# Kernel optimization log

Measured on AMD Instinct MI355X. Metric: run time of the kernel, lower is better.

## Reference

```python
import jax, jax.numpy as jnp
import numpy as np

RADIUS = 0.2
NSAMPLE = 32
GROUPS = 4
EPS = 1e-5


def group_norm(x, gamma, beta):
    # x: [B, C, *spatial]; normalize per (batch, group) over channels-in-group + spatial
    B, C = x.shape[0], x.shape[1]
    rest = x.shape[2:]
    xr = x.reshape(B, GROUPS, -1)
    mean = xr.mean(-1, keepdims=True)
    var = xr.var(-1, keepdims=True)
    xr = (xr - mean) * jax.lax.rsqrt(var + EPS)
    x = xr.reshape((B, C) + rest)
    bshape = (1, C) + (1,) * len(rest)
    return x * gamma.reshape(bshape) + beta.reshape(bshape)


def ball_query(pos_t):
    # pos_t: [B, N, 3] -> idx [B, N, NSAMPLE] (query points == all points)
    N = pos_t.shape[1]
    sq = jnp.sum(pos_t * pos_t, axis=-1)  # [B, N]
    d = sq[:, :, None] + sq[:, None, :] - 2.0 * jnp.einsum('bnc,bmc->bnm', pos_t, pos_t)
    ar = jnp.arange(N, dtype=jnp.int32)
    gi = jnp.where(d > RADIUS * RADIUS, N, ar[None, None, :])  # [B, S, N]
    gi = jnp.sort(gi, axis=-1)[:, :, :NSAMPLE]  # ascending in-ball indices first
    first = gi[:, :, :1]
    gi = jnp.where(gi == N, first, gi)  # pad with first neighbor
    return gi


def setup_inputs() -> dict:
    key = jax.random.key(0)
    ks = jax.random.split(key, 6)
    B, C, N = 2, 64, 4096
    M = 4 * C  # mid channels
    return {
        'x': jax.random.normal(ks[0], (B, C, N), jnp.float32),
        'pos': jax.random.uniform(ks[1], (B, 3, N), jnp.float32),
        'w1': jax.random.normal(ks[2], (M, C), jnp.float32) * 0.05,
        'b1': jnp.zeros((M,), jnp.float32),
        'g1': jnp.ones((M,), jnp.float32),
        'be1': jnp.zeros((M,), jnp.float32),
        'wd': 1.0 + jax.random.normal(ks[3], (M,), jnp.float32) * 0.05,
        'gd': jnp.ones((M,), jnp.float32),
        'bed': jnp.zeros((M,), jnp.float32),
        'w2': jax.random.normal(ks[4], (C, M), jnp.float32) * 0.05,
        'b2': jnp.zeros((C,), jnp.float32),
        'g2': jnp.ones((C,), jnp.float32),
        'be2': jnp.zeros((C,), jnp.float32),
    }


def reference(x, pos, w1, b1, g1, be1, wd, gd, bed, w2, b2, g2, be2):
    # x: [B, C, N], pos: [B, 3, N]
    pos_t = jnp.transpose(pos, (0, 2, 1))  # [B, N, 3]
    idx = ball_query(pos_t)  # [B, N, K]

    # conv1 (1x1) -> GroupNorm -> GELU
    h = jnp.einsum('mc,bcn->bmn', w1, x) + b1[None, :, None]
    h = jax.nn.gelu(group_norm(h, g1, be1), approximate=False)  # [B, M, N]

    # gather neighbors: feats [B, N, M] indexed by idx [B, N, K]
    feats = jnp.transpose(h, (0, 2, 1))
    grouped = jax.vmap(lambda f, i: f[i])(feats, idx)  # [B, N, K, M]
    grouped = jnp.transpose(grouped, (0, 3, 1, 2))  # [B, M, N, K]

    # depthwise 1x1 conv (per-channel scale, no bias) -> GroupNorm -> max-pool over K -> GELU
    grouped = grouped * wd[None, :, None, None]
    grouped = group_norm(grouped, gd, bed)
    h2 = jax.nn.gelu(jnp.max(grouped, axis=-1), approximate=False)  # [B, M, N]

    # conv2 (1x1) -> GroupNorm -> residual
    out = jnp.einsum('cm,bmn->bcn', w2, h2) + b2[None, :, None]
    out = group_norm(out, g2, be2)
    return out + x
```

## Files before the change

kernel.cpp:

```cpp
#include <hip/hip_runtime.h>
#include <hip/hip_fp16.h>
#include <math.h>

#define BB 2
#define CC 64
#define NN 4096
#define MM 256
#define KK 32
#define GG 4
#define EPSF 1e-5f

__device__ __forceinline__ float gelu_exact(float x) {
    return 0.5f * x * (1.0f + erff(x * 0.70710678118654752f));
}

__device__ __forceinline__ unsigned pkmax(unsigned a, unsigned b) {
    unsigned d;
    asm volatile("v_pk_max_f16 %0, %1, %2" : "=v"(d) : "v"(a), "v"(b));
    return d;
}
__device__ __forceinline__ unsigned pkmin(unsigned a, unsigned b) {
    unsigned d;
    asm volatile("v_pk_min_f16 %0, %1, %2" : "=v"(d) : "v"(a), "v"(b));
    return d;
}
__device__ __forceinline__ unsigned selpair(unsigned mx, unsigned mn, float g0, float g1) {
    unsigned lo = (g0 >= 0.f) ? (mx & 0x0000FFFFu) : (mn & 0x0000FFFFu);
    unsigned hi = (g1 >= 0.f) ? (mx & 0xFFFF0000u) : (mn & 0xFFFF0000u);
    return lo | hi;
}

__global__ void k_init(double* st) {
    int t = threadIdx.x;
    if (t < 48) st[t] = 0.0;
}

__global__ void k_mlp1(const float* __restrict__ x, const float* __restrict__ w1,
                       const float* __restrict__ b1, float* __restrict__ h, double* st1) {
    __shared__ float xs[64 * 128];
    __shared__ float w1t[64 * 32];
    __shared__ float r1[4], r2[4];

    int bx = blockIdx.x;
    int nt = bx & 31, mt = (bx >> 5) & 7, b = bx >> 8;
    int n0 = nt * 128, m0 = mt * 32;
    int t = threadIdx.x;

    {
        int nq = t & 31, ch = t >> 5;
        #pragma unroll
        for (int p = 0; p < 8; p++) {
            int c = p * 8 + ch;
            float4 v = *(const float4*)&x[((size_t)(b * CC + c)) * NN + n0 + nq * 4];
            *(float4*)&xs[c * 128 + nq * 4] = v;
        }
    }
    {
        #pragma unroll
        for (int p = 0; p < 2; p++) {
            int idx = p * 256 + t;
            int m = idx >> 4, cq = idx & 15;
            float4 v = *(const float4*)&w1[(m0 + m) * CC + cq * 4];
            w1t[(cq * 4 + 0) * 32 + m] = v.x;
            w1t[(cq * 4 + 1) * 32 + m] = v.y;
            w1t[(cq * 4 + 2) * 32 + m] = v.z;
            w1t[(cq * 4 + 3) * 32 + m] = v.w;
        }
    }
    __syncthreads();

    int nq = t & 31;
    int mseg = t >> 5;
    float o[4][4];
    #pragma unroll
    for (int i = 0; i < 4; i++)
        #pragma unroll
        for (int j = 0; j < 4; j++) o[i][j] = 0.f;

    for (int c = 0; c < 64; c++) {
        float4 xv = *(float4*)&xs[c * 128 + nq * 4];
        float4 wv = *(float4*)&w1t[c * 32 + mseg * 4];
        o[0][0] = fmaf(wv.x, xv.x, o[0][0]); o[0][1] = fmaf(wv.x, xv.y, o[0][1]);
        o[0][2] = fmaf(wv.x, xv.z, o[0][2]); o[0][3] = fmaf(wv.x, xv.w, o[0][3]);
        o[1][0] = fmaf(wv.y, xv.x, o[1][0]); o[1][1] = fmaf(wv.y, xv.y, o[1][1]);
        o[1][2] = fmaf(wv.y, xv.z, o[1][2]); o[1][3] = fmaf(wv.y, xv.w, o[1][3]);
        o[2][0] = fmaf(wv.z, xv.x, o[2][0]); o[2][1] = fmaf(wv.z, xv.y, o[2][1]);
        o[2][2] = fmaf(wv.z, xv.z, o[2][2]); o[2][3] = fmaf(wv.z, xv.w, o[2][3]);
        o[3][0] = fmaf(wv.w, xv.x, o[3][0]); o[3][1] = fmaf(wv.w, xv.y, o[3][1]);
        o[3][2] = fmaf(wv.w, xv.z, o[3][2]); o[3][3] = fmaf(wv.w, xv.w, o[3][3]);
    }

    float s1 = 0.f, s2 = 0.f;
    #pragma unroll
    for (int mi = 0; mi < 4; mi++) {
        int m = m0 + mseg * 4 + mi;
        float bv = b1[m];
        float4 r;
        r.x = o[mi][0] + bv; r.y = o[mi][1] + bv;
        r.z = o[mi][2] + bv; r.w = o[mi][3] + bv;
        *(float4*)&h[((size_t)(b * MM + m)) * NN + n0 + nq * 4] = r;
        s1 += r.x + r.y + r.z + r.w;
        s2 = fmaf(r.x, r.x, s2); s2 = fmaf(r.y, r.y, s2);
        s2 = fmaf(r.z, r.z, s2); s2 = fmaf(r.w, r.w, s2);
    }
    for (int off = 32; off; off >>= 1) {
        s1 += __shfl_down(s1, off, 64);
        s2 += __shfl_down(s2, off, 64);
    }
    int w = t >> 6, l = t & 63;
    if (l == 0) { r1[w] = s1; r2[w] = s2; }
    __syncthreads();
    if (t == 0) {
        float ts1 = r1[0] + r1[1] + r1[2] + r1[3];
        float ts2 = r2[0] + r2[1] + r2[2] + r2[3];
        int g = m0 >> 6;
        atomicAdd(&st1[(b * GG + g) * 2 + 0], (double)ts1);
        atomicAdd(&st1[(b * GG + g) * 2 + 1], (double)ts2);
    }
}

__global__ void k_gn1t(const float* __restrict__ h, const float* __restrict__ g1,
                       const float* __restrict__ be1, const float* __restrict__ wd,
                       const double* __restrict__ st1, __half* __restrict__ pH,
                       float* __restrict__ R) {
    int n0 = blockIdx.x * 64;
    int m0 = blockIdx.y * 64;
    int b  = blockIdx.z;
    int g  = m0 >> 6;
    double s1 = st1[(b * GG + g) * 2 + 0];
    double s2 = st1[(b * GG + g) * 2 + 1];
    const double cnt = 64.0 * 4096.0;
    double mean_d = s1 / cnt;
    double var_d  = s2 / cnt - mean_d * mean_d;
    float mean = (float)mean_d;
    float rstd = rsqrtf((float)var_d + EPSF);

    __shared__ float tile[64 * 65];
    int t = threadIdx.x;
    int nq = t & 15, mr = t >> 4;
    #pragma unroll
    for (int pp = 0; pp < 4; pp++) {
        int row = pp * 16 + mr;
        int m = m0 + row;
        float a = rstd * g1[m];
        float cc2 = be1[m] - mean * a;
        float wdm = wd[m];
        float4 hv = *(const float4*)&h[((size_t)(b * MM + m)) * NN + n0 + nq * 4];
        tile[row * 65 + nq * 4 + 0] = gelu_exact(fmaf(hv.x, a, cc2)) * wdm;
        tile[row * 65 + nq * 4 + 1] = gelu_exact(fmaf(hv.y, a, cc2)) * wdm;
        tile[row * 65 + nq * 4 + 2] = gelu_exact(fmaf(hv.z, a, cc2)) * wdm;
        tile[row * 65 + nq * 4 + 3] = gelu_exact(fmaf(hv.w, a, cc2)) * wdm;
    }
    __syncthreads();
    #pragma unroll
    for (int pp = 0; pp < 4; pp++) {
        int id = pp * 256 + t;
        int nl = id >> 4, mq = id & 15;
        float a0 = tile[(mq * 4 + 0) * 65 + nl];
        float a1 = tile[(mq * 4 + 1) * 65 + nl];
        float a2 = tile[(mq * 4 + 2) * 65 + nl];
        float a3 = tile[(mq * 4 + 3) * 65 + nl];
        __half2 hA = __float22half2_rn(make_float2(a0, a1));
        __half2 hB = __float22half2_rn(make_float2(a2, a3));
        uint2 st8;
        st8.x = *(unsigned*)&hA; st8.y = *(unsigned*)&hB;
        *(uint2*)((char*)pH + ((((size_t)(b * NN) + n0 + nl)) << 9) + (m0 + mq * 4) * 2) = st8;
        float2 fa = __half22float2(hA);
        float2 fb = __half22float2(hB);
        float t1 = fa.x + fa.y + fb.x + fb.y;
        float t2 = fa.x * fa.x + fa.y * fa.y + fb.x * fb.x + fb.y * fb.y;
        #pragma unroll
        for (int off = 8; off; off >>= 1) {
            t1 += __shfl_down(t1, off, 16);
            t2 += __shfl_down(t2, off, 16);
        }
        if ((t & 15) == 0) {
            float* rr = &R[((size_t)(b * NN) + n0 + nl) * 8];
            rr[g]     = t1;
            rr[4 + g] = t2;
        }
    }
}

__global__ void k_ballq(const float* __restrict__ pos, int* __restrict__ idx) {
    int wid  = blockIdx.x * 4 + (threadIdx.x >> 6);
    int lane = threadIdx.x & 63;
    int b = wid >> 12;
    int n = wid & 4095;
    const float* px = pos + b * 3 * NN;
    const float* py = px + NN;
    const float* pz = py + NN;
    float qx = px[n], qy = py[n], qz = pz[n];
    float qsq = qx*qx + qy*qy + qz*qz;
    int* row = idx + (b * NN + n) * KK;

    int found = 0;
    int first = -1;
    const float R2 = 0.04f;
    for (int m0 = 0; m0 < NN && found < KK; m0 += 64) {
        int m = m0 + lane;
        float ax = px[m], ay = py[m], az = pz[m];
        float msq = ax*ax + ay*ay + az*az;
        float dot = qx*ax + qy*ay + qz*az;
        float d = qsq + msq - 2.0f * dot;
        bool hit = !(d > R2);
        unsigned long long mask = __ballot(hit);
        if (first < 0 && mask) first = m0 + (__ffsll((long long)mask) - 1);
        unsigned long long lt = (lane == 0) ? 0ULL : (mask & ((1ULL << lane) - 1ULL));
        int posh = __popcll(lt);
        if (hit && (found + posh) < KK) row[found + posh] = m;
        found += __popcll(mask);
        if (found > KK) found = KK;
    }
    if (lane < KK && lane >= found) row[lane] = first;
}

__global__ void k_gstats(const int* __restrict__ idx, const float* __restrict__ R,
                         double* st2) {
    __shared__ float acc[8];
    int t = threadIdx.x;
    if (t < 8) acc[t] = 0.f;
    __syncthreads();
    int hw = t >> 5, cl = t & 31;
    int pbase = blockIdx.x * 32;
    int b = pbase >> 12;
    float s[8];
    #pragma unroll
    for (int c = 0; c < 8; c++) s[c] = 0.f;
    #pragma unroll
    for (int it = 0; it < 4; it++) {
        int pt = pbase + it * 8 + hw;
        int j = idx[pt * KK + cl];
        const float* rr = &R[((size_t)(b * NN) + j) * 8];
        float4 ra = *(const float4*)rr;
        float4 rb = *(const float4*)(rr + 4);
        s[0] += ra.x; s[1] += ra.y; s[2] += ra.z; s[3] += ra.w;
        s[4] += rb.x; s[5] += rb.y; s[6] += rb.z; s[7] += rb.w;
    }
    #pragma unroll
    for (int off = 16; off; off >>= 1) {
        #pragma unroll
        for (int c = 0; c < 8; c++) s[c] += __shfl_down(s[c], off, 32);
    }
    if (cl == 0) {
        #pragma unroll
        for (int c = 0; c < 8; c++) atomicAdd(&acc[c], s[c]);
    }
    __syncthreads();
    if (t < 8) {
        int g = t & 3, isR2 = t >> 2;
        atomicAdd(&st2[(b * GG + g) * 2 + isR2], (double)acc[t]);
    }
}

__global__ __launch_bounds__(256)
void k_gather(const __half* __restrict__ pH, const int* __restrict__ idx,
              const float* __restrict__ gd, __half* __restrict__ pselH) {
    int t = threadIdx.x;
    int w = t >> 6, l = t & 63;
    int gn = blockIdx.x * 4 + w;
    int b = gn >> 12;
    int h = l >> 5, cl = l & 31;
    int myidx = idx[gn * KK + cl];
    const char* pb = (const char*)(pH + (size_t)b * NN * 256);
    int laneoff = cl * 16;

    unsigned vmax0 = 0xFC00FC00u, vmax1 = 0xFC00FC00u, vmax2 = 0xFC00FC00u, vmax3 = 0xFC00FC00u;
    unsigned vmin0 = 0x7C007C00u, vmin1 = 0x7C007C00u, vmin2 = 0x7C007C00u, vmin3 = 0x7C007C00u;

    #pragma unroll
    for (int k = 0; k < 16; k++) {
        int ja = __shfl(myidx, 2 * k, 64);
        int jb = __shfl(myidx, 2 * k + 1, 64);
        int j = h ? jb : ja;
        uint4 raw = *(const uint4*)(pb + (((size_t)j) << 9) + laneoff);
        vmax0 = pkmax(vmax0, raw.x); vmin0 = pkmin(vmin0, raw.x);
        vmax1 = pkmax(vmax1, raw.y); vmin1 = pkmin(vmin1, raw.y);
        vmax2 = pkmax(vmax2, raw.z); vmin2 = pkmin(vmin2, raw.z);
        vmax3 = pkmax(vmax3, raw.w); vmin3 = pkmin(vmin3, raw.w);
    }
    vmax0 = pkmax(vmax0, (unsigned)__shfl_xor((int)vmax0, 32, 64));
    vmax1 = pkmax(vmax1, (unsigned)__shfl_xor((int)vmax1, 32, 64));
    vmax2 = pkmax(vmax2, (unsigned)__shfl_xor((int)vmax2, 32, 64));
    vmax3 = pkmax(vmax3, (unsigned)__shfl_xor((int)vmax3, 32, 64));
    vmin0 = pkmin(vmin0, (unsigned)__shfl_xor((int)vmin0, 32, 64));
    vmin1 = pkmin(vmin1, (unsigned)__shfl_xor((int)vmin1, 32, 64));
    vmin2 = pkmin(vmin2, (unsigned)__shfl_xor((int)vmin2, 32, 64));
    vmin3 = pkmin(vmin3, (unsigned)__shfl_xor((int)vmin3, 32, 64));

    if (h == 0) {
        const float4* g4 = (const float4*)gd;
        float4 gA = g4[cl * 2], gB = g4[cl * 2 + 1];
        uint4 out;
        out.x = selpair(vmax0, vmin0, gA.x, gA.y);
        out.y = selpair(vmax1, vmin1, gA.z, gA.w);
        out.z = selpair(vmax2, vmin2, gB.x, gB.y);
        out.w = selpair(vmax3, vmin3, gB.z, gB.w);
        *(uint4*)((char*)pselH + (((size_t)gn) << 9) + laneoff) = out;
    }
}

__global__ __launch_bounds__(256, 4)
void k_mlp2(const __half* __restrict__ pselH,
            const float* __restrict__ w2, const float* __restrict__ b2,
            const float* __restrict__ gd, const float* __restrict__ bed,
            const double* __restrict__ st2, float* __restrict__ oraw, double* st3) {
    __shared__ float w2s[64 * 257];

    int t = threadIdx.x;
    int w = t >> 6, l = t & 63;
    int b  = blockIdx.x >> 7;
    int n0 = (blockIdx.x & 127) * 32 + w * 8;

    #pragma unroll
    for (int p = 0; p < 16; p++) {
        int i = p * 256 + t;
        int c = i >> 6, mq = i & 63;
        float4 v = ((const float4*)w2)[i];
        float* dst = &w2s[c * 257 + mq * 4];
        dst[0] = v.x; dst[1] = v.y; dst[2] = v.z; dst[3] = v.w;
    }

    const double cnt2 = 64.0 * 4096.0 * 32.0;
    int g = l >> 4;
    double m_ = st2[(b * GG + g) * 2 + 0] / cnt2;
    double v_ = st2[(b * GG + g) * 2 + 1] / cnt2 - m_ * m_;
    float mean = (float)m_;
    float rstd = rsqrtf((float)v_ + EPSF);
    float4 gd4  = ((const float4*)gd)[l];
    float4 bed4 = ((const float4*)bed)[l];
    float ax = rstd * gd4.x, ay = rstd * gd4.y, az = rstd * gd4.z, aw = rstd * gd4.w;
    float cx = bed4.x - mean * ax, cy = bed4.y - mean * ay;
    float cz = bed4.z - mean * az, cw = bed4.w - mean * aw;

    float4 h2r[8];
    #pragma unroll
    for (int j = 0; j < 8; j++) {
        uint2 raw = *(const uint2*)((const char*)pselH +
                     ((((size_t)(b * NN)) + n0 + j) << 9) + l * 8);
        float2 fa = __half22float2(*(__half2*)&raw.x);
        float2 fb = __half22float2(*(__half2*)&raw.y);
        h2r[j].x = gelu_exact(fmaf(fa.x, ax, cx));
        h2r[j].y = gelu_exact(fmaf(fa.y, ay, cy));
        h2r[j].z = gelu_exact(fmaf(fb.x, az, cz));
        h2r[j].w = gelu_exact(fmaf(fb.y, aw, cw));
    }
    __syncthreads();

    const float* w2l = &w2s[l * 257];
    float acc[8];
    #pragma unroll
    for (int j = 0; j < 8; j++) acc[j] = 0.f;

    #pragma unroll 8
    for (int mq = 0; mq < 64; mq++) {
        float w0 = w2l[4 * mq + 0];
        float w1_ = w2l[4 * mq + 1];
        float w2_ = w2l[4 * mq + 2];
        float w3_ = w2l[4 * mq + 3];
        #pragma unroll
        for (int j = 0; j < 8; j++) {
            acc[j] = fmaf(w0,  __int_as_float(__builtin_amdgcn_readlane(__float_as_int(h2r[j].x), mq)), acc[j]);
            acc[j] = fmaf(w1_, __int_as_float(__builtin_amdgcn_readlane(__float_as_int(h2r[j].y), mq)), acc[j]);
            acc[j] = fmaf(w2_, __int_as_float(__builtin_amdgcn_readlane(__float_as_int(h2r[j].z), mq)), acc[j]);
            acc[j] = fmaf(w3_, __int_as_float(__builtin_amdgcn_readlane(__float_as_int(h2r[j].w), mq)), acc[j]);
        }
    }

    float bias = b2[l];
    float so1 = 0.f, so2 = 0.f;
    #pragma unroll
    for (int j = 0; j < 8; j++) {
        acc[j] += bias;
        so1 += acc[j];
        so2 = fmaf(acc[j], acc[j], so2);
    }
    float* dst = &oraw[((size_t)(b * CC) + l) * NN + n0];
    *(float4*)&dst[0] = make_float4(acc[0], acc[1], acc[2], acc[3]);
    *(float4*)&dst[4] = make_float4(acc[4], acc[5], acc[6], acc[7]);

    so1 += __shfl_down(so1, 8, 16); so2 += __shfl_down(so2, 8, 16);
    so1 += __shfl_down(so1, 4, 16); so2 += __shfl_down(so2, 4, 16);
    so1 += __shfl_down(so1, 2, 16); so2 += __shfl_down(so2, 2, 16);
    so1 += __shfl_down(so1, 1, 16); so2 += __shfl_down(so2, 1, 16);
    if ((l & 15) == 0) {
        int g3 = l >> 4;
        atomicAdd(&st3[(b * GG + g3) * 2 + 0], (double)so1);
        atomicAdd(&st3[(b * GG + g3) * 2 + 1], (double)so2);
    }
}

__global__ void k_final(const float* __restrict__ oraw, const float* __restrict__ x,
                        const float* __restrict__ g2, const float* __restrict__ be2,
                        const double* __restrict__ st3, float* __restrict__ out) {
    int i4 = blockIdx.x * 256 + threadIdx.x;
    int base = i4 * 4;
    int c = (base >> 12) & 63;
    int b = base >> 18;
    int g = c >> 4;
    const double cnt = 16.0 * 4096.0;
    double mean_d = st3[(b * GG + g) * 2 + 0] / cnt;
    double var_d  = st3[(b * GG + g) * 2 + 1] / cnt - mean_d * mean_d;
    float mean = (float)mean_d;
    float rstd = rsqrtf((float)var_d + EPSF);
    float sc = rstd * g2[c];
    float ad = be2[c] - mean * sc;
    float4 o = ((const float4*)oraw)[i4];
    float4 xv = ((const float4*)x)[i4];
    float4 r;
    r.x = fmaf(o.x, sc, ad) + xv.x;
    r.y = fmaf(o.y, sc, ad) + xv.y;
    r.z = fmaf(o.z, sc, ad) + xv.z;
    r.w = fmaf(o.w, sc, ad) + xv.w;
    ((float4*)out)[i4] = r;
}

extern "C" void kernel_launch(void* const* d_in, const int* in_sizes, int n_in,
                              void* d_out, int out_size, void* d_ws, size_t ws_size,
                              hipStream_t stream) {
    const float* x   = (const float*)d_in[0];
    const float* pos = (const float*)d_in[1];
    const float* w1  = (const float*)d_in[2];
    const float* b1  = (const float*)d_in[3];
    const float* g1  = (const float*)d_in[4];
    const float* be1 = (const float*)d_in[5];
    const float* wd  = (const float*)d_in[6];
    const float* gd  = (const float*)d_in[7];
    const float* bed = (const float*)d_in[8];
    const float* w2  = (const float*)d_in[9];
    const float* b2  = (const float*)d_in[10];
    const float* g2  = (const float*)d_in[11];
    const float* be2 = (const float*)d_in[12];
    float* out = (float*)d_out;

    char* wsb = (char*)d_ws;
    float*  h     = (float*)wsb;
    __half* pH    = (__half*)(wsb + 8388608);
    __half* pselH = (__half*)(wsb + 12582912);
    float*  oraw  = (float*)(wsb + 16777216);
    int*    idx   = (int*)(wsb + 18874368);
    float*  R     = (float*)(wsb + 19922944);
    double* st    = (double*)(wsb + 20185088);
    double* st1 = st;
    double* st2 = st + 16;
    double* st3 = st + 32;

    k_init<<<1, 64, 0, stream>>>(st);
    k_mlp1<<<512, 256, 0, stream>>>(x, w1, b1, h, st1);
    k_gn1t<<<dim3(64, 4, 2), 256, 0, stream>>>(h, g1, be1, wd, st1, pH, R);
    k_ballq<<<2048, 256, 0, stream>>>(pos, idx);
    k_gstats<<<256, 256, 0, stream>>>(idx, R, st2);
    k_gather<<<2048, 256, 0, stream>>>(pH, idx, gd, pselH);
    k_mlp2<<<256, 256, 0, stream>>>(pselH, w2, b2, gd, bed, st2, oraw, st3);
    k_final<<<512, 256, 0, stream>>>(oraw, x, g2, be2, st3, out);
}
```

Measured before the change: 175.0 us.

## Replace double atomics with per-block partials and fuse gather statistics into gather kernel

Removes the init kernel and all global double atomicAdds for the three GroupNorm statistics. Each producer block now writes float partial sums, and the consumer kernel reduces them itself. The separate gather-stats kernel is folded into the gather kernel, where the otherwise idle second half-wave computes per-point sums of R. mlp2 now processes 4 points per wave with twice as many blocks. In exchange, every mlp2 block redundantly reduces all 4096 Rp partials for its batch, and k_final re-reduces the Op partials in every block.

```diff
diff --git a/kernel.cpp b/kernel.cpp
--- a/kernel.cpp
+++ b/kernel.cpp
@@ -29,14 +29,13 @@
     unsigned hi = (g1 >= 0.f) ? (mx & 0xFFFF0000u) : (mn & 0xFFFF0000u);
     return lo | hi;
 }
-
-__global__ void k_init(double* st) {
-    int t = threadIdx.x;
-    if (t < 48) st[t] = 0.0;
+__device__ __forceinline__ float bcast_lane(float v, int lane) {
+    return __int_as_float(__builtin_amdgcn_readlane(__float_as_int(v), lane));
 }
 
 __global__ void k_mlp1(const float* __restrict__ x, const float* __restrict__ w1,
-                       const float* __restrict__ b1, float* __restrict__ h, double* st1) {
+                       const float* __restrict__ b1, float* __restrict__ h,
+                       float2* __restrict__ Mp) {
     __shared__ float xs[64 * 128];
     __shared__ float w1t[64 * 32];
     __shared__ float r1[4], r2[4];
@@ -111,32 +110,41 @@
     if (l == 0) { r1[w] = s1; r2[w] = s2; }
     __syncthreads();
     if (t == 0) {
-        float ts1 = r1[0] + r1[1] + r1[2] + r1[3];
-        float ts2 = r2[0] + r2[1] + r2[2] + r2[3];
-        int g = m0 >> 6;
-        atomicAdd(&st1[(b * GG + g) * 2 + 0], (double)ts1);
-        atomicAdd(&st1[(b * GG + g) * 2 + 1], (double)ts2);
+        Mp[bx] = make_float2(r1[0] + r1[1] + r1[2] + r1[3],
+                             r2[0] + r2[1] + r2[2] + r2[3]);
     }
 }
 
 __global__ void k_gn1t(const float* __restrict__ h, const float* __restrict__ g1,
                        const float* __restrict__ be1, const float* __restrict__ wd,
-                       const double* __restrict__ st1, __half* __restrict__ pH,
+                       const float2* __restrict__ Mp, __half* __restrict__ pH,
                        float* __restrict__ R) {
+    __shared__ float tile[64 * 65];
+    __shared__ float mv[2];
     int n0 = blockIdx.x * 64;
     int m0 = blockIdx.y * 64;
     int b  = blockIdx.z;
-    int g  = m0 >> 6;
-    double s1 = st1[(b * GG + g) * 2 + 0];
-    double s2 = st1[(b * GG + g) * 2 + 1];
-    const double cnt = 64.0 * 4096.0;
-    double mean_d = s1 / cnt;
-    double var_d  = s2 / cnt - mean_d * mean_d;
-    float mean = (float)mean_d;
-    float rstd = rsqrtf((float)var_d + EPSF);
-
-    __shared__ float tile[64 * 65];
+    int g  = blockIdx.y;
     int t = threadIdx.x;
+
+    if (t < 64) {
+        float2 p2 = Mp[b * 256 + g * 64 + t];
+        float s1 = p2.x, s2 = p2.y;
+        for (int off = 32; off; off >>= 1) {
+            s1 += __shfl_down(s1, off, 64);
+            s2 += __shfl_down(s2, off, 64);
+        }
+        if (t == 0) {
+            const double cnt = 64.0 * 4096.0;
+            double md = (double)s1 / cnt;
+            double vd = (double)s2 / cnt - md * md;
+            mv[0] = (float)md;
+            mv[1] = rsqrtf((float)vd + EPSF);
+        }
+    }
+    __syncthreads();
+    float mean = mv[0], rstd = mv[1];
+
     int nq = t & 15, mr = t >> 4;
     #pragma unroll
     for (int pp = 0; pp < 4; pp++) {
@@ -215,52 +223,15 @@
     if (lane < KK && lane >= found) row[lane] = first;
 }
 
-__global__ void k_gstats(const int* __restrict__ idx, const float* __restrict__ R,
-                         double* st2) {
-    __shared__ float acc[8];
-    int t = threadIdx.x;
-    if (t < 8) acc[t] = 0.f;
-    __syncthreads();
-    int hw = t >> 5, cl = t & 31;
-    int pbase = blockIdx.x * 32;
-    int b = pbase >> 12;
-    float s[8];
-    #pragma unroll
-    for (int c = 0; c < 8; c++) s[c] = 0.f;
-    #pragma unroll
-    for (int it = 0; it < 4; it++) {
-        int pt = pbase + it * 8 + hw;
-        int j = idx[pt * KK + cl];
-        const float* rr = &R[((size_t)(b * NN) + j) * 8];
-        float4 ra = *(const float4*)rr;
-        float4 rb = *(const float4*)(rr + 4);
-        s[0] += ra.x; s[1] += ra.y; s[2] += ra.z; s[3] += ra.w;
-        s[4] += rb.x; s[5] += rb.y; s[6] += rb.z; s[7] += rb.w;
-    }
-    #pragma unroll
-    for (int off = 16; off; off >>= 1) {
-        #pragma unroll
-        for (int c = 0; c < 8; c++) s[c] += __shfl_down(s[c], off, 32);
-    }
-    if (cl == 0) {
-        #pragma unroll
-        for (int c = 0; c < 8; c++) atomicAdd(&acc[c], s[c]);
-    }
-    __syncthreads();
-    if (t < 8) {
-        int g = t & 3, isR2 = t >> 2;
-        atomicAdd(&st2[(b * GG + g) * 2 + isR2], (double)acc[t]);
-    }
-}
-
 __global__ __launch_bounds__(256)
-void k_gather(const __half* __restrict__ pH, const int* __restrict__ idx,
-              const float* __restrict__ gd, __half* __restrict__ pselH) {
-    int t = threadIdx.x;
-    int w = t >> 6, l = t & 63;
+void k_qgather(const __half* __restrict__ pH, const int* __restrict__ idx,
+               const float* __restrict__ R, const float* __restrict__ gd,
+               __half* __restrict__ pselH, float* __restrict__ Rp) {
+    int t = threadIdx.x, w = t >> 6, l = t & 63;
     int gn = blockIdx.x * 4 + w;
     int b = gn >> 12;
-    int h = l >> 5, cl = l & 31;
+
+    int hh = l >> 5, cl = l & 31;
     int myidx = idx[gn * KK + cl];
     const char* pb = (const char*)(pH + (size_t)b * NN * 256);
     int laneoff = cl * 16;
@@ -272,7 +243,7 @@
     for (int k = 0; k < 16; k++) {
         int ja = __shfl(myidx, 2 * k, 64);
         int jb = __shfl(myidx, 2 * k + 1, 64);
-        int j = h ? jb : ja;
+        int j = hh ? jb : ja;
         uint4 raw = *(const uint4*)(pb + (((size_t)j) << 9) + laneoff);
         vmax0 = pkmax(vmax0, raw.x); vmin0 = pkmin(vmin0, raw.x);
         vmax1 = pkmax(vmax1, raw.y); vmin1 = pkmin(vmin1, raw.y);
@@ -288,7 +259,7 @@
     vmin2 = pkmin(vmin2, (unsigned)__shfl_xor((int)vmin2, 32, 64));
     vmin3 = pkmin(vmin3, (unsigned)__shfl_xor((int)vmin3, 32, 64));
 
-    if (h == 0) {
+    if (hh == 0) {
         const float4* g4 = (const float4*)gd;
         float4 gA = g4[cl * 2], gB = g4[cl * 2 + 1];
         uint4 out;
@@ -297,20 +268,37 @@
         out.z = selpair(vmax2, vmin2, gB.x, gB.y);
         out.w = selpair(vmax3, vmin3, gB.z, gB.w);
         *(uint4*)((char*)pselH + (((size_t)gn) << 9) + laneoff) = out;
+    } else {
+        const float* rr = &R[((size_t)(b * NN) + myidx) * 8];
+        float4 ra = *(const float4*)rr;
+        float4 rb = *(const float4*)(rr + 4);
+        float s[8] = {ra.x, ra.y, ra.z, ra.w, rb.x, rb.y, rb.z, rb.w};
+        #pragma unroll
+        for (int off = 16; off; off >>= 1) {
+            #pragma unroll
+            for (int c = 0; c < 8; c++) s[c] += __shfl_down(s[c], off, 32);
+        }
+        if (cl == 0) {
+            float4* rp = (float4*)&Rp[(size_t)gn * 8];
+            rp[0] = make_float4(s[0], s[1], s[2], s[3]);
+            rp[1] = make_float4(s[4], s[5], s[6], s[7]);
+        }
     }
 }
 
 __global__ __launch_bounds__(256, 4)
-void k_mlp2(const __half* __restrict__ pselH,
+void k_mlp2(const __half* __restrict__ pselH, const float* __restrict__ Rp,
             const float* __restrict__ w2, const float* __restrict__ b2,
             const float* __restrict__ gd, const float* __restrict__ bed,
-            const double* __restrict__ st2, float* __restrict__ oraw, double* st3) {
+            float* __restrict__ oraw, float* __restrict__ Op) {
     __shared__ float w2s[64 * 257];
+    __shared__ float sw[4][8];
+    __shared__ float sA[4][4], sB[4][4];
 
     int t = threadIdx.x;
     int w = t >> 6, l = t & 63;
-    int b  = blockIdx.x >> 7;
-    int n0 = (blockIdx.x & 127) * 32 + w * 8;
+    int b  = blockIdx.x >> 8;
+    int n0 = (blockIdx.x & 255) * 16 + w * 4;
 
     #pragma unroll
     for (int p = 0; p < 16; p++) {
@@ -321,10 +309,34 @@
         dst[0] = v.x; dst[1] = v.y; dst[2] = v.z; dst[3] = v.w;
     }
 
+    {
+        const float4* rp = (const float4*)(Rp + (size_t)b * NN * 8);
+        float s[8] = {0.f, 0.f, 0.f, 0.f, 0.f, 0.f, 0.f, 0.f};
+        #pragma unroll
+        for (int r = 0; r < 16; r++) {
+            float4 ra = rp[(t * 16 + r) * 2];
+            float4 rb = rp[(t * 16 + r) * 2 + 1];
+            s[0] += ra.x; s[1] += ra.y; s[2] += ra.z; s[3] += ra.w;
+            s[4] += rb.x; s[5] += rb.y; s[6] += rb.z; s[7] += rb.w;
+        }
+        #pragma unroll
+        for (int off = 32; off; off >>= 1) {
+            #pragma unroll
+            for (int c = 0; c < 8; c++) s[c] += __shfl_down(s[c], off, 64);
+        }
+        if (l == 0) {
+            #pragma unroll
+            for (int c = 0; c < 8; c++) sw[w][c] = s[c];
+        }
+    }
+    __syncthreads();
+
+    int g = l >> 4;
+    double s1 = (double)sw[0][g] + sw[1][g] + sw[2][g] + sw[3][g];
+    double s2 = (double)sw[0][4 + g] + sw[1][4 + g] + sw[2][4 + g] + sw[3][4 + g];
     const double cnt2 = 64.0 * 4096.0 * 32.0;
-    int g = l >> 4;
-    double m_ = st2[(b * GG + g) * 2 + 0] / cnt2;
-    double v_ = st2[(b * GG + g) * 2 + 1] / cnt2 - m_ * m_;
+    double m_ = s1 / cnt2;
+    double v_ = s2 / cnt2 - m_ * m_;
     float mean = (float)m_;
     float rstd = rsqrtf((float)v_ + EPSF);
     float4 gd4  = ((const float4*)gd)[l];
@@ -333,9 +345,9 @@
     float cx = bed4.x - mean * ax, cy = bed4.y - mean * ay;
     float cz = bed4.z - mean * az, cw = bed4.w - mean * aw;
 
-    float4 h2r[8];
-    #pragma unroll
-    for (int j = 0; j < 8; j++) {
+    float4 h2r[4];
+    #pragma unroll
+    for (int j = 0; j < 4; j++) {
         uint2 raw = *(const uint2*)((const char*)pselH +
                      ((((size_t)(b * NN)) + n0 + j) << 9) + l * 8);
         float2 fa = __half22float2(*(__half2*)&raw.x);
@@ -345,62 +357,81 @@
         h2r[j].z = gelu_exact(fmaf(fb.x, az, cz));
         h2r[j].w = gelu_exact(fmaf(fb.y, aw, cw));
     }
-    __syncthreads();
 
     const float* w2l = &w2s[l * 257];
-    float acc[8];
-    #pragma unroll
-    for (int j = 0; j < 8; j++) acc[j] = 0.f;
-
+    float acc[4] = {0.f, 0.f, 0.f, 0.f};
     #pragma unroll 8
     for (int mq = 0; mq < 64; mq++) {
-        float w0 = w2l[4 * mq + 0];
+        float w0  = w2l[4 * mq + 0];
         float w1_ = w2l[4 * mq + 1];
         float w2_ = w2l[4 * mq + 2];
         float w3_ = w2l[4 * mq + 3];
         #pragma unroll
-        for (int j = 0; j < 8; j++) {
-            acc[j] = fmaf(w0,  __int_as_float(__builtin_amdgcn_readlane(__float_as_int(h2r[j].x), mq)), acc[j]);
-            acc[j] = fmaf(w1_, __int_as_float(__builtin_amdgcn_readlane(__float_as_int(h2r[j].y), mq)), acc[j]);
-            acc[j] = fmaf(w2_, __int_as_float(__builtin_amdgcn_readlane(__float_as_int(h2r[j].z), mq)), acc[j]);
-            acc[j] = fmaf(w3_, __int_as_float(__builtin_amdgcn_readlane(__float_as_int(h2r[j].w), mq)), acc[j]);
+        for (int j = 0; j < 4; j++) {
+            acc[j] = fmaf(w0,  bcast_lane(h2r[j].x, mq), acc[j]);
+            acc[j] = fmaf(w1_, bcast_lane(h2r[j].y, mq), acc[j]);
+            acc[j] = fmaf(w2_, bcast_lane(h2r[j].z, mq), acc[j]);
+            acc[j] = fmaf(w3_, bcast_lane(h2r[j].w, mq), acc[j]);
         }
     }
 
     float bias = b2[l];
     float so1 = 0.f, so2 = 0.f;
     #pragma unroll
-    for (int j = 0; j < 8; j++) {
+    for (int j = 0; j < 4; j++) {
         acc[j] += bias;
         so1 += acc[j];
         so2 = fmaf(acc[j], acc[j], so2);
     }
-    float* dst = &oraw[((size_t)(b * CC) + l) * NN + n0];
-    *(float4*)&dst[0] = make_float4(acc[0], acc[1], acc[2], acc[3]);
-    *(float4*)&dst[4] = make_float4(acc[4], acc[5], acc[6], acc[7]);
+    *(float4*)&oraw[((size_t)(b * CC) + l) * NN + n0] =
+        make_float4(acc[0], acc[1], acc[2], acc[3]);
 
     so1 += __shfl_down(so1, 8, 16); so2 += __shfl_down(so2, 8, 16);
     so1 += __shfl_down(so1, 4, 16); so2 += __shfl_down(so2, 4, 16);
     so1 += __shfl_down(so1, 2, 16); so2 += __shfl_down(so2, 2, 16);
     so1 += __shfl_down(so1, 1, 16); so2 += __shfl_down(so2, 1, 16);
-    if ((l & 15) == 0) {
-        int g3 = l >> 4;
-        atomicAdd(&st3[(b * GG + g3) * 2 + 0], (double)so1);
-        atomicAdd(&st3[(b * GG + g3) * 2 + 1], (double)so2);
+    if ((l & 15) == 0) { sA[w][l >> 4] = so1; sB[w][l >> 4] = so2; }
+    __syncthreads();
+    if (t < 8) {
+        int is2 = t >> 2, gg = t & 3;
+        float v = is2 ? (sB[0][gg] + sB[1][gg] + sB[2][gg] + sB[3][gg])
+                      : (sA[0][gg] + sA[1][gg] + sA[2][gg] + sA[3][gg]);
+        Op[blockIdx.x * 8 + t] = v;
     }
 }
 
 __global__ void k_final(const float* __restrict__ oraw, const float* __restrict__ x,
                         const float* __restrict__ g2, const float* __restrict__ be2,
-                        const double* __restrict__ st3, float* __restrict__ out) {
-    int i4 = blockIdx.x * 256 + threadIdx.x;
+                        const float* __restrict__ Op, float* __restrict__ out) {
+    __shared__ float fw[4][8];
+    int t = threadIdx.x;
+    int i4 = blockIdx.x * 256 + t;
     int base = i4 * 4;
+    int b = base >> 18;
+
+    {
+        const float4* rp = (const float4*)(Op + ((size_t)b * 256 + t) * 8);
+        float4 ra = rp[0], rb = rp[1];
+        float s[8] = {ra.x, ra.y, ra.z, ra.w, rb.x, rb.y, rb.z, rb.w};
+        #pragma unroll
+        for (int off = 32; off; off >>= 1) {
+            #pragma unroll
+            for (int c = 0; c < 8; c++) s[c] += __shfl_down(s[c], off, 64);
+        }
+        if ((t & 63) == 0) {
+            #pragma unroll
+            for (int c = 0; c < 8; c++) fw[t >> 6][c] = s[c];
+        }
+    }
+    __syncthreads();
+
     int c = (base >> 12) & 63;
-    int b = base >> 18;
     int g = c >> 4;
+    double s1 = (double)fw[0][g] + fw[1][g] + fw[2][g] + fw[3][g];
+    double s2 = (double)fw[0][4 + g] + fw[1][4 + g] + fw[2][4 + g] + fw[3][4 + g];
     const double cnt = 16.0 * 4096.0;
-    double mean_d = st3[(b * GG + g) * 2 + 0] / cnt;
-    double var_d  = st3[(b * GG + g) * 2 + 1] / cnt - mean_d * mean_d;
+    double mean_d = s1 / cnt;
+    double var_d  = s2 / cnt - mean_d * mean_d;
     float mean = (float)mean_d;
     float rstd = rsqrtf((float)var_d + EPSF);
     float sc = rstd * g2[c];
@@ -440,17 +471,14 @@
     float*  oraw  = (float*)(wsb + 16777216);
     int*    idx   = (int*)(wsb + 18874368);
     float*  R     = (float*)(wsb + 19922944);
-    double* st    = (double*)(wsb + 20185088);
-    double* st1 = st;
-    double* st2 = st + 16;
-    double* st3 = st + 32;
-
-    k_init<<<1, 64, 0, stream>>>(st);
-    k_mlp1<<<512, 256, 0, stream>>>(x, w1, b1, h, st1);
-    k_gn1t<<<dim3(64, 4, 2), 256, 0, stream>>>(h, g1, be1, wd, st1, pH, R);
+    float*  Rp    = (float*)(wsb + 20185088);
+    float2* Mp    = (float2*)(wsb + 20447232);
+    float*  Op    = (float*)(wsb + 20451328);
+
+    k_mlp1<<<512, 256, 0, stream>>>(x, w1, b1, h, Mp);
+    k_gn1t<<<dim3(64, 4, 2), 256, 0, stream>>>(h, g1, be1, wd, Mp, pH, R);
     k_ballq<<<2048, 256, 0, stream>>>(pos, idx);
-    k_gstats<<<256, 256, 0, stream>>>(idx, R, st2);
-    k_gather<<<2048, 256, 0, stream>>>(pH, idx, gd, pselH);
-    k_mlp2<<<256, 256, 0, stream>>>(pselH, w2, b2, gd, bed, st2, oraw, st3);
-    k_final<<<512, 256, 0, stream>>>(oraw, x, g2, be2, st3, out);
-}
+    k_qgather<<<2048, 256, 0, stream>>>(pH, idx, R, gd, pselH, Rp);
+    k_mlp2<<<512, 256, 0, stream>>>(pselH, Rp, w2, b2, gd, bed, oraw, Op);
+    k_final<<<512, 256, 0, stream>>>(oraw, x, g2, be2, Op, out);
+}
```

New measurement: 155.7 us. 11.0% less time.
